# Kernel tuning notes

Hardware: AMD Instinct MI355X
Metric: run time of the kernel (lower is better)

The kernel has to match this reference:

```python
import jax, jax.numpy as jnp
import numpy as np

NEG_SLOPE = 0.1  # negative slope of LeakyReLU in Conv3dReLU/Conv2dReLU


def setup_inputs() -> dict:
    key = jax.random.key(0)
    ks = jax.random.split(key, 16)
    B, C, PREV, N, M1, M2 = 2, 16, 16, 16384, 4096, 4096
    D1, CORR, FILT = 4, 15, 15          # d1 = d+1; (r+1)^d1 - r^d1 with r=1
    CO0, CO1 = 32, 32                    # num_corr_output
    O0, O1 = 64, 64                      # num_output
    CIN = 2 * C + PREV                   # corr_conv input channels

    feat1 = jax.random.normal(ks[0], (B, C, M1), jnp.float32)
    feat2 = jax.random.normal(ks[1], (B, C, M2), jnp.float32)
    prev_corr_feat = jax.random.normal(ks[2], (B, PREV, N), jnp.float32)
    barycentric1 = jax.random.uniform(ks[3], (B, D1, N), jnp.float32)
    # lattice_offset1: batch-offset flattened indices into [0, B*(M1+1)); value -1+1=0 is the pad slot
    local = jax.random.randint(ks[4], (B, D1, N), 0, M1)
    lattice_offset1 = local + (jnp.arange(B, dtype=jnp.int64) * (M1 + 1))[:, None, None]
    pc1_corr_indices = jax.random.randint(ks[5], (B, CORR, M1), -1, M1).astype(jnp.int64)
    pc2_corr_indices = jax.random.randint(ks[6], (B, FILT, CORR, M1), -1, M2).astype(jnp.int64)

    s = 0.05
    cw0 = jax.random.normal(ks[7], (CO0, CIN, CORR), jnp.float32) * s   # Conv3d (1,corr_size,1)
    cb0 = jax.random.normal(ks[8], (CO0,), jnp.float32) * s
    cw1 = jax.random.normal(ks[9], (CO1, CO0), jnp.float32) * s        # Conv3d 1x1x1
    cb1 = jax.random.normal(ks[10], (CO1,), jnp.float32) * s
    bw0 = jax.random.normal(ks[11], (O0, CO1, FILT), jnp.float32) * s  # Conv2d (filter_size,1)
    bb0 = jax.random.normal(ks[12], (O0,), jnp.float32) * s
    bw1 = jax.random.normal(ks[13], (O1, O0), jnp.float32) * s         # Conv2d 1x1 (no relu)
    bb1 = jax.random.normal(ks[14], (O1,), jnp.float32) * s

    return {
        "feat1": feat1, "feat2": feat2, "prev_corr_feat": prev_corr_feat,
        "barycentric1": barycentric1,
        "cw0": cw0, "cb0": cb0, "cw1": cw1, "cb1": cb1,
        "bw0": bw0, "bb0": bb0, "bw1": bw1, "bb1": bb1,
        "lattice_offset1": lattice_offset1,
        "pc1_corr_indices": pc1_corr_indices,
        "pc2_corr_indices": pc2_corr_indices,
        "max_hash_cnt1": M1, "max_hash_cnt2": M2,
    }


def reference(feat1, feat2, prev_corr_feat, barycentric1,
              cw0, cb0, cw1, cb1, bw0, bb0, bw1, bb1,
              lattice_offset1, pc1_corr_indices, pc2_corr_indices,
              max_hash_cnt1, max_hash_cnt2):
    B, C, M1 = feat1.shape
    PREV = prev_corr_feat.shape[1]

    # ---- splat prev_corr_feat onto lattice vertices (scatter-add) ----
    flat_idx = (lattice_offset1 + 1).reshape(-1)                      # (B*d1*N,)
    # (B, PREV, d1, N) -> (B, d1, N, PREV) -> (B*d1*N, PREV)
    vals = (barycentric1[:, None, :, :] * prev_corr_feat[:, :, None, :])
    vals = vals.transpose(0, 2, 3, 1).reshape(-1, PREV)
    prev_splat = jax.ops.segment_sum(vals, flat_idx, num_segments=B * (M1 + 1))
    prev_splat = prev_splat.reshape(B, M1 + 1, PREV).transpose(0, 2, 1)  # (B, PREV, M1+1)

    # use_norm: normalize by splatted barycentric mass
    ones_splat = jax.ops.segment_sum(barycentric1.reshape(-1), flat_idx,
                                     num_segments=B * (M1 + 1)).reshape(B, M1 + 1)
    prev_splat = prev_splat * (1.0 / (ones_splat + 1e-5))[:, None, :]

    # ---- prepend zero pad slot (index 0 catches -1 neighbor indices) ----
    splat1 = jnp.concatenate([prev_splat, jnp.pad(feat1, ((0, 0), (0, 0), (1, 0)))], axis=1)  # (B, PREV+C, M1+1)
    splat2 = jnp.pad(feat2, ((0, 0), (0, 0), (1, 0)))                                          # (B, C, M2+1)

    # ---- irregular gathers ----
    g1 = jax.vmap(lambda s, i: s[:, i])(splat1, pc1_corr_indices + 1)   # (B, PREV+C, corr, M1)
    g2 = jax.vmap(lambda s, i: s[:, i])(splat2, pc2_corr_indices + 1)   # (B, C, filt, corr, M1)
    FILT = g2.shape[2]
    g1b = jnp.broadcast_to(g1[:, :, None], (B, g1.shape[1], FILT, g1.shape[2], M1))
    combined = jnp.concatenate([g1b, g2], axis=1)                       # (B, 2C+PREV, filt, corr, M1)

    # ---- corr_conv: Conv3d(1,corr,1)+LeakyReLU, then 1x1x1+LeakyReLU ----
    x = jnp.einsum('bifkn,oik->bofn', combined, cw0) + cb0[None, :, None, None]
    x = jax.nn.leaky_relu(x, NEG_SLOPE)
    x = jnp.einsum('bcfn,oc->bofn', x, cw1) + cb1[None, :, None, None]
    x = jax.nn.leaky_relu(x, NEG_SLOPE)

    # ---- blur_conv: Conv2d(filt,1)+LeakyReLU, then 1x1 (last_relu=False) ----
    y = jnp.einsum('bcfn,ocf->bon', x, bw0) + bb0[None, :, None]
    y = jax.nn.leaky_relu(y, NEG_SLOPE)
    y = jnp.einsum('bcn,oc->bon', y, bw1) + bb1[None, :, None]
    return y
```

## Files before the change

kernel.cpp:

```cpp
#include <hip/hip_runtime.h>
#include <hip/hip_bf16.h>

namespace {

constexpr int B     = 2;
constexpr int C     = 16;
constexpr int PREVC = 16;
constexpr int NPTS  = 16384;
constexpr int M1    = 4096;
constexpr int D1    = 4;
constexpr int CORR  = 15;
constexpr int FILT  = 15;
constexpr int CIN   = 48;
constexpr int CO0   = 32;
constexpr int O1    = 64;
constexpr int MS    = M1 + 1;
constexpr int NSLOT = B * MS;
constexpr int NPAIR = B * D1 * NPTS;
constexpr int BCAP  = 64;
constexpr int GSTR  = 240;
constexpr float NEG = 0.1f;

constexpr size_t OFF_SP1   = 0;
constexpr size_t SZ_SP1    = (size_t)NSLOT * 32;
constexpr size_t OFF_SP2   = OFF_SP1 + SZ_SP1;
constexpr size_t SZ_SP2    = (size_t)NSLOT * 16;
constexpr size_t OFF_P     = OFF_SP2 + SZ_SP2;
constexpr size_t SZ_PQ     = (size_t)B * CORR * MS * 32 / 2;
constexpr size_t OFF_Q     = OFF_P + SZ_PQ;
constexpr size_t OFF_CWT   = OFF_Q + SZ_PQ;
constexpr size_t SZ_CWT    = (size_t)CORR * CIN * 32;
constexpr size_t OFF_W0R   = OFF_CWT + SZ_CWT;
constexpr size_t SZ_W0R    = 512 * 64;
constexpr size_t OFF_PREVT = OFF_W0R + SZ_W0R;
constexpr size_t SZ_PREVT  = (size_t)B * NPTS * 16;
constexpr size_t OFF_CNT   = OFF_PREVT + SZ_PREVT;
constexpr size_t SZ_CNT    = 8208;
constexpr size_t OFF_REC   = OFF_CNT + SZ_CNT;
constexpr size_t SZ_REC    = (size_t)NSLOT * BCAP;
constexpr size_t OFF_GT    = OFF_REC + SZ_REC;
constexpr size_t SZ_GT     = (size_t)B * M1 * GSTR;

__device__ __forceinline__ float leaky(float v) { return v > 0.f ? v : NEG * v; }
__device__ __forceinline__ float bflo(unsigned u) { return __uint_as_float(u << 16); }
__device__ __forceinline__ float bfhi(unsigned u) { return __uint_as_float(u & 0xffff0000u); }

__global__ __launch_bounds__(256) void k_pre(const int* __restrict__ lo,
                                             const float* __restrict__ prev,
                                             const float* __restrict__ cw0,
                                             const float* __restrict__ bw0,
                                             const int* __restrict__ pc1,
                                             const int* __restrict__ pc2,
                                             int* __restrict__ counts,
                                             int* __restrict__ rec,
                                             float* __restrict__ prevT,
                                             float* __restrict__ cwT,
                                             float* __restrict__ W0r,
                                             unsigned int* __restrict__ gT) {
  int bx = blockIdx.x, tid = threadIdx.x;
  if (bx < 512) {
    int t = bx * 256 + tid;
    int slot = lo[t] + 1;
    int pos = atomicAdd(counts + slot, 1);
    if (pos < BCAP) rec[slot * BCAP + pos] = t;
  } else if (bx < 1024) {
    __shared__ float tile[16][65];
    int bb = bx - 512;
    int b = bb >> 8, n0 = (bb & 255) * 64;
    for (int e = tid; e < 1024; e += 256) {
      int ln = e & 63, r = e >> 6;
      tile[r][ln] = prev[((size_t)b * PREVC + r) * NPTS + n0 + ln];
    }
    __syncthreads();
    for (int e = tid; e < 1024; e += 256) {
      int c = e & 15, nn = e >> 4;
      prevT[((size_t)b * NPTS + n0 + nn) * 16 + c] = tile[c][nn];
    }
  } else if (bx < 1243) {
    int e = (bx - 1024) * 256 + tid;
    if (e < CORR * CIN * 32) {
      int o = e & 31, i = (e >> 5) % CIN, k = e / (CIN * 32);
      cwT[e] = cw0[((size_t)o * CIN + i) * CORR + k];
    }
    int e2 = e - CORR * CIN * 32;
    if (e2 >= 0 && e2 < 512 * 64) {
      int o3 = e2 & 63, cf = e2 >> 6, c = cf >> 4, f = cf & 15;
      W0r[e2] = (f < FILT) ? bw0[((size_t)o3 * CO0 + c) * FILT + f] : 0.f;
    }
  } else {
    __shared__ int tile[16][65];
    int t = bx - 1243;
    int n0 = (t & 63) * 64;
    int rest = t >> 6;
    int b = rest & 1;
    int rt = rest >> 1;
    const int* src; int r0, nr, doff;
    if (rt < 15) { src = pc2 + (size_t)b * FILT * CORR * M1; r0 = rt * 16;
                   nr = min(16, FILT * CORR - r0); doff = 0; }
    else         { src = pc1 + (size_t)b * CORR * M1; r0 = 0; nr = CORR; doff = 225; }
    for (int e = tid; e < nr * 64; e += 256) {
      int ln = e & 63, r = e >> 6;
      tile[r][ln] = src[(size_t)(r0 + r) * M1 + n0 + ln] + 1;
    }
    __syncthreads();
    for (int e = tid; e < 1024; e += 256) {
      int rr = e & 15, nn = e >> 4;
      if (rr < nr)
        gT[((size_t)b * M1 + n0 + nn) * GSTR + doff + r0 + rr] =
            (unsigned int)(tile[rr][nn] * 64);
    }
  }
}

__global__ __launch_bounds__(256) void k_sum(const int* __restrict__ rec,
                                             const int* __restrict__ counts,
                                             const float* __restrict__ bary,
                                             const float* __restrict__ prevT,
                                             const float* __restrict__ feat1,
                                             const float* __restrict__ feat2,
                                             float* __restrict__ splat1,
                                             float* __restrict__ splat2) {
  int tid = threadIdx.x;
  int s = blockIdx.x * 4 + (tid >> 6);
  if (s >= NSLOT) return;
  int lane = tid & 63, c = lane & 15, g = lane >> 4;
  int cnt = min(counts[s], BCAP);
  const int* bucket = rec + (size_t)s * BCAP;
  float acc = 0.f, wsum = 0.f;
  for (int e = g; e < cnt; e += 4) {
    int t = bucket[e];
    float w = bary[t];
    int n = t & (NPTS - 1);
    int b = t >> 16;
    acc += w * prevT[((size_t)b * NPTS + n) * 16 + c];
    wsum += w;
  }
  acc  += __shfl_down(acc, 32);  acc  += __shfl_down(acc, 16);
  wsum += __shfl_down(wsum, 32); wsum += __shfl_down(wsum, 16);
  if (lane < 16) {
    int m = s % MS, b2 = s / MS;
    float scale = 1.f / (wsum + 1e-5f);
    splat1[(size_t)s * 32 + c] = acc * scale;
    float f1 = (m == 0) ? 0.f : feat1[((size_t)b2 * C + c) * M1 + (m - 1)];
    splat1[(size_t)s * 32 + 16 + c] = f1;
    float f2 = (m == 0) ? 0.f : feat2[((size_t)b2 * C + c) * M1 + (m - 1)];
    splat2[(size_t)s * 16 + c] = f2;
  }
}

__global__ __launch_bounds__(256) void k_pq(const float* __restrict__ sp1,
                                            const float* __restrict__ sp2,
                                            const float* __restrict__ cwT,
                                            __hip_bfloat16* __restrict__ Pt,
                                            __hip_bfloat16* __restrict__ Qt) {
  __shared__ float wk[CIN][33];
  int k = blockIdx.y, b = blockIdx.z;
  int tid = threadIdx.x;
  int m = blockIdx.x * 16 + (tid >> 4);
  int o2 = tid & 15;
  for (int e = tid; e < CIN * 32; e += 256)
    wk[e >> 5][e & 31] = cwT[(size_t)k * CIN * 32 + e];
  __syncthreads();
  if (m >= MS) return;
  const float* s1 = sp1 + ((size_t)b * MS + m) * 32;
  const float* s2 = sp2 + ((size_t)b * MS + m) * 16;
  int oa = o2 * 2, ob = oa + 1;
  float q0 = 0, q1 = 0, p0 = 0, p1 = 0;
#pragma unroll
  for (int i4 = 0; i4 < 8; ++i4) {
    float4 s = *(const float4*)(s1 + i4 * 4);
    q0 += s.x * wk[i4*4+0][oa] + s.y * wk[i4*4+1][oa] + s.z * wk[i4*4+2][oa] + s.w * wk[i4*4+3][oa];
    q1 += s.x * wk[i4*4+0][ob] + s.y * wk[i4*4+1][ob] + s.z * wk[i4*4+2][ob] + s.w * wk[i4*4+3][ob];
  }
#pragma unroll
  for (int i4 = 0; i4 < 4; ++i4) {
    float4 s = *(const float4*)(s2 + i4 * 4);
    p0 += s.x * wk[32+i4*4+0][oa] + s.y * wk[32+i4*4+1][oa] + s.z * wk[32+i4*4+2][oa] + s.w * wk[32+i4*4+3][oa];
    p1 += s.x * wk[32+i4*4+0][ob] + s.y * wk[32+i4*4+1][ob] + s.z * wk[32+i4*4+2][ob] + s.w * wk[32+i4*4+3][ob];
  }
  size_t base = ((size_t)(b * CORR + k) * MS + m) * 32;
  __hip_bfloat162 qq, pp;
  qq.x = __float2bfloat16(q0); qq.y = __float2bfloat16(q1);
  pp.x = __float2bfloat16(p0); pp.y = __float2bfloat16(p1);
  *reinterpret_cast<__hip_bfloat162*>(Qt + base + oa) = qq;
  *reinterpret_cast<__hip_bfloat162*>(Pt + base + oa) = pp;
}

__global__ __launch_bounds__(256, 4) void k_gather(const __hip_bfloat16* __restrict__ Pt,
                                                   const __hip_bfloat16* __restrict__ Qt,
                                                   const unsigned int* __restrict__ gT,
                                                   const float* __restrict__ cw1,
                                                   const float* __restrict__ cb0,
                                                   const float* __restrict__ cb1,
                                                   const float* __restrict__ W0r,
                                                   const float* __restrict__ bb0,
                                                   const float* __restrict__ bw1,
                                                   const float* __restrict__ bb1,
                                                   float* __restrict__ out) {
  __shared__ __attribute__((aligned(16))) char smem[19072];
  unsigned int* idxs = (unsigned int*)smem;
  float* parts       = (float*)smem;
  float* p1s         = (float*)(smem + 4096);
  float* xls         = (float*)(smem + 4608);
  float* wch         = (float*)(smem + 4608);
  __hip_bfloat16* hT = (__hip_bfloat16*)(smem + 13824);
  float* y0s         = (float*)(smem + 17984);

  int bid = blockIdx.x;
  int b = (bid >> 2) & 1;
  int r = bid & 3, x = bid >> 3;
  int n0 = (r << 10) | (x << 2);
  int pt0 = (b << 12) | n0;
  int tid = threadIdx.x;

  for (int e = tid; e < 240; e += 256) {
    int pl = e / 60, d = e - pl * 60;
    ((uint4*)(idxs + pl * GSTR))[d] =
        ((const uint4*)(gT + (size_t)(pt0 + pl) * GSTR))[d];
  }
  __syncthreads();

  int pl = tid >> 6, lane = tid & 63;

  {
    int f = lane >> 2, o4 = lane & 3;
    const char* base = (const char*)((f < CORR ? Pt : Qt) + (size_t)b * CORR * MS * 32);
    const unsigned int* ip = idxs + pl * GSTR + (f < CORR ? f * CORR : 225);
    unsigned int lo = (unsigned int)(o4 * 16);
    float a[8] = {};
#pragma unroll
    for (int k = 0; k < CORR; ++k) {
      unsigned int off = ip[k] + (unsigned int)(k * MS * 64) + lo;
      uint4 d = *(const uint4*)(base + off);
      a[0] += bflo(d.x); a[1] += bfhi(d.x);
      a[2] += bflo(d.y); a[3] += bfhi(d.y);
      a[4] += bflo(d.z); a[5] += bfhi(d.z);
      a[6] += bflo(d.w); a[7] += bfhi(d.w);
    }
    if (f == CORR) {
#pragma unroll
      for (int j = 0; j < 8; ++j)
        p1s[pl * 32 + o4 * 8 + j] = a[j] + cb0[o4 * 8 + j];
    }
    __syncthreads();
    if (f < CORR) {
#pragma unroll
      for (int j = 0; j < 8; ++j)
        xls[pl * 576 + f * 36 + o4 * 8 + j] = leaky(a[j] + p1s[pl * 32 + o4 * 8 + j]);
    }
  }
  __syncthreads();

  {
    int o = lane & 31, fh = lane >> 5;
    const float* wrow = cw1 + o * CO0;
    float bias = cb1[o];
    float h[8];
#pragma unroll
    for (int j = 0; j < 8; ++j) {
      float hh = bias;
#pragma unroll
      for (int c4 = 0; c4 < 8; ++c4) {
        float4 xv = *(const float4*)&xls[pl * 576 + (fh * 8 + j) * 36 + c4 * 4];
        float4 w  = *(const float4*)(wrow + c4 * 4);
        hh += w.x * xv.x + w.y * xv.y + w.z * xv.z + w.w * xv.w;
      }
      h[j] = leaky(hh);
    }
    if (fh == 1) h[7] = 0.f;
    union { __hip_bfloat16 hb[8]; uint4 u; } pk;
#pragma unroll
    for (int j = 0; j < 8; ++j) pk.hb[j] = __float2bfloat16(h[j]);
    *(uint4*)(hT + pl * 520 + o * 16 + fh * 8) = pk.u;
  }

  int og = tid & 15, bpl = (tid >> 4) & 3, rep = tid >> 6;
  float acc[4] = {};
  for (int kc = 0; kc < 512; kc += 32) {
    __syncthreads();
    for (int e = tid; e < 512; e += 256) {
      int rr = e >> 4, c4 = e & 15;
      *(float4*)&wch[rr * 68 + c4 * 4] = *(const float4*)(W0r + (size_t)(kc + rr) * 64 + c4 * 4);
    }
    __syncthreads();
#pragma unroll
    for (int i = 0; i < 8; ++i) {
      int kk = rep + i * 4;
      float hv = __bfloat162float(hT[bpl * 520 + kc + kk]);
      float4 w = *(const float4*)&wch[kk * 68 + og * 4];
      acc[0] += w.x * hv; acc[1] += w.y * hv; acc[2] += w.z * hv; acc[3] += w.w * hv;
    }
  }
  __syncthreads();
  *(float4*)&parts[((rep * 4 + bpl) * 16 + og) * 4] = make_float4(acc[0], acc[1], acc[2], acc[3]);
  __syncthreads();

  {
    int ypl = tid & 3, yo3 = tid >> 2;
    int og2 = yo3 >> 2, comp = yo3 & 3;
    float y0 = bb0[yo3];
#pragma unroll
    for (int rp = 0; rp < 4; ++rp)
      y0 += parts[((rp * 4 + ypl) * 16 + og2) * 4 + comp];
    y0s[ypl * 68 + yo3] = leaky(y0);
  }
  __syncthreads();

  {
    int fpl = tid & 3, fo1 = tid >> 2;
    const float* w1row = bw1 + fo1 * 64;
    float y1 = bb1[fo1];
#pragma unroll
    for (int c4 = 0; c4 < 16; ++c4) {
      float4 w = *(const float4*)(w1row + c4 * 4);
      y1 += w.x * y0s[fpl * 68 + c4 * 4 + 0] + w.y * y0s[fpl * 68 + c4 * 4 + 1] +
            w.z * y0s[fpl * 68 + c4 * 4 + 2] + w.w * y0s[fpl * 68 + c4 * 4 + 3];
    }
    out[((size_t)(b * O1 + fo1)) * M1 + n0 + fpl] = y1;
  }
}

}

extern "C" void kernel_launch(void* const* d_in, const int* in_sizes, int n_in,
                              void* d_out, int out_size, void* d_ws, size_t ws_size,
                              hipStream_t stream) {
  const float* feat1 = (const float*)d_in[0];
  const float* feat2 = (const float*)d_in[1];
  const float* prev  = (const float*)d_in[2];
  const float* bary  = (const float*)d_in[3];
  const float* cw0   = (const float*)d_in[4];
  const float* cb0   = (const float*)d_in[5];
  const float* cw1   = (const float*)d_in[6];
  const float* cb1   = (const float*)d_in[7];
  const float* bw0   = (const float*)d_in[8];
  const float* bb0   = (const float*)d_in[9];
  const float* bw1   = (const float*)d_in[10];
  const float* bb1   = (const float*)d_in[11];
  const int* lo  = (const int*)d_in[12];
  const int* pc1 = (const int*)d_in[13];
  const int* pc2 = (const int*)d_in[14];

  float* ws = (float*)d_ws;
  float* splat1 = ws + OFF_SP1;
  float* splat2 = ws + OFF_SP2;
  __hip_bfloat16* Pt = (__hip_bfloat16*)(ws + OFF_P);
  __hip_bfloat16* Qt = (__hip_bfloat16*)(ws + OFF_Q);
  float* cwT   = ws + OFF_CWT;
  float* W0r   = ws + OFF_W0R;
  float* prevT = ws + OFF_PREVT;
  int* counts  = (int*)(ws + OFF_CNT);
  int* rec     = (int*)(ws + OFF_REC);
  unsigned int* gT = (unsigned int*)(ws + OFF_GT);
  float* out   = (float*)d_out;

  hipMemsetAsync(counts, 0, NSLOT * sizeof(int), stream);

  hipLaunchKernelGGL(k_pre, dim3(1243 + 2048), dim3(256), 0, stream,
                     lo, prev, cw0, bw0, pc1, pc2, counts, rec, prevT, cwT, W0r, gT);
  hipLaunchKernelGGL(k_sum, dim3((NSLOT + 3) / 4), dim3(256), 0, stream,
                     rec, counts, bary, prevT, feat1, feat2, splat1, splat2);
  hipLaunchKernelGGL(k_pq, dim3((MS + 15) / 16, CORR, B), dim3(256), 0, stream,
                     splat1, splat2, cwT, Pt, Qt);
  hipLaunchKernelGGL(k_gather, dim3(B * M1 / 4), dim3(256), 0, stream,
                     Pt, Qt, gT, cw1, cb0, cb1, W0r, bb0, bw1, bb1, out);
}
```

Baseline: 112.8 us.

## Shrink gather indices to 16-bit, loop corr in k_pq, read W0r directly

Gather indices are stored as 16-bit values and scaled by 64 in the gather kernel instead of being pre-scaled 32-bit, which halves the index table traffic. k_pq now stages each block's splat rows in shared memory once and loops over all CORR weight slices, rather than launching one block per slice and re-reading the splat rows each time. The blur-conv GEMV in k_gather drops its chunked shared-memory staging of W0r with its barriers and reads weights straight from global memory (cache) with vectorized bf16 unpacking. In exchange, k_pq has fewer, longer blocks and the weight reads in k_gather depend on cache hits.

```diff
diff --git a/kernel.cpp b/kernel.cpp
--- a/kernel.cpp
+++ b/kernel.cpp
@@ -39,7 +39,7 @@
 constexpr size_t OFF_REC   = OFF_CNT + SZ_CNT;
 constexpr size_t SZ_REC    = (size_t)NSLOT * BCAP;
 constexpr size_t OFF_GT    = OFF_REC + SZ_REC;
-constexpr size_t SZ_GT     = (size_t)B * M1 * GSTR;
+constexpr size_t SZ_GT     = (size_t)B * M1 * GSTR / 2;
 
 __device__ __forceinline__ float leaky(float v) { return v > 0.f ? v : NEG * v; }
 __device__ __forceinline__ float bflo(unsigned u) { return __uint_as_float(u << 16); }
@@ -56,7 +56,7 @@
                                              float* __restrict__ prevT,
                                              float* __restrict__ cwT,
                                              float* __restrict__ W0r,
-                                             unsigned int* __restrict__ gT) {
+                                             unsigned short* __restrict__ gT) {
   int bx = blockIdx.x, tid = threadIdx.x;
   if (bx < 512) {
     int t = bx * 256 + tid;
@@ -107,7 +107,7 @@
       int rr = e & 15, nn = e >> 4;
       if (rr < nr)
         gT[((size_t)b * M1 + n0 + nn) * GSTR + doff + r0 + rr] =
-            (unsigned int)(tile[rr][nn] * 64);
+            (unsigned short)tile[rr][nn];
     }
   }
 }
@@ -153,42 +153,54 @@
                                             const float* __restrict__ cwT,
                                             __hip_bfloat16* __restrict__ Pt,
                                             __hip_bfloat16* __restrict__ Qt) {
+  __shared__ float s1s[16][33];
+  __shared__ float s2s[16][17];
   __shared__ float wk[CIN][33];
-  int k = blockIdx.y, b = blockIdx.z;
+  int b = blockIdx.y;
   int tid = threadIdx.x;
-  int m = blockIdx.x * 16 + (tid >> 4);
-  int o2 = tid & 15;
-  for (int e = tid; e < CIN * 32; e += 256)
-    wk[e >> 5][e & 31] = cwT[(size_t)k * CIN * 32 + e];
-  __syncthreads();
-  if (m >= MS) return;
-  const float* s1 = sp1 + ((size_t)b * MS + m) * 32;
-  const float* s2 = sp2 + ((size_t)b * MS + m) * 16;
+  int m0 = blockIdx.x * 16;
+  int mm = tid >> 4, o2 = tid & 15;
+  int m = m0 + mm;
+  for (int e = tid; e < 512; e += 256) {
+    int r = e >> 5, i = e & 31;
+    s1s[r][i] = (m0 + r < MS) ? sp1[((size_t)b * MS + m0 + r) * 32 + i] : 0.f;
+  }
+  {
+    int r = tid >> 4, i = tid & 15;
+    s2s[r][i] = (m0 + r < MS) ? sp2[((size_t)b * MS + m0 + r) * 16 + i] : 0.f;
+  }
+  bool valid = (m < MS);
   int oa = o2 * 2, ob = oa + 1;
-  float q0 = 0, q1 = 0, p0 = 0, p1 = 0;
-#pragma unroll
-  for (int i4 = 0; i4 < 8; ++i4) {
-    float4 s = *(const float4*)(s1 + i4 * 4);
-    q0 += s.x * wk[i4*4+0][oa] + s.y * wk[i4*4+1][oa] + s.z * wk[i4*4+2][oa] + s.w * wk[i4*4+3][oa];
-    q1 += s.x * wk[i4*4+0][ob] + s.y * wk[i4*4+1][ob] + s.z * wk[i4*4+2][ob] + s.w * wk[i4*4+3][ob];
-  }
-#pragma unroll
-  for (int i4 = 0; i4 < 4; ++i4) {
-    float4 s = *(const float4*)(s2 + i4 * 4);
-    p0 += s.x * wk[32+i4*4+0][oa] + s.y * wk[32+i4*4+1][oa] + s.z * wk[32+i4*4+2][oa] + s.w * wk[32+i4*4+3][oa];
-    p1 += s.x * wk[32+i4*4+0][ob] + s.y * wk[32+i4*4+1][ob] + s.z * wk[32+i4*4+2][ob] + s.w * wk[32+i4*4+3][ob];
-  }
-  size_t base = ((size_t)(b * CORR + k) * MS + m) * 32;
-  __hip_bfloat162 qq, pp;
-  qq.x = __float2bfloat16(q0); qq.y = __float2bfloat16(q1);
-  pp.x = __float2bfloat16(p0); pp.y = __float2bfloat16(p1);
-  *reinterpret_cast<__hip_bfloat162*>(Qt + base + oa) = qq;
-  *reinterpret_cast<__hip_bfloat162*>(Pt + base + oa) = pp;
+  for (int k = 0; k < CORR; ++k) {
+    __syncthreads();
+    for (int e = tid; e < CIN * 32; e += 256)
+      wk[e >> 5][e & 31] = cwT[(size_t)k * CIN * 32 + e];
+    __syncthreads();
+    if (valid) {
+      float q0 = 0, q1 = 0, p0 = 0, p1 = 0;
+#pragma unroll
+      for (int i = 0; i < 32; ++i) {
+        float s = s1s[mm][i];
+        q0 += s * wk[i][oa]; q1 += s * wk[i][ob];
+      }
+#pragma unroll
+      for (int i = 0; i < 16; ++i) {
+        float s = s2s[mm][i];
+        p0 += s * wk[32 + i][oa]; p1 += s * wk[32 + i][ob];
+      }
+      size_t base = ((size_t)(b * CORR + k) * MS + m) * 32;
+      __hip_bfloat162 qq, pp;
+      qq.x = __float2bfloat16(q0); qq.y = __float2bfloat16(q1);
+      pp.x = __float2bfloat16(p0); pp.y = __float2bfloat16(p1);
+      *reinterpret_cast<__hip_bfloat162*>(Qt + base + oa) = qq;
+      *reinterpret_cast<__hip_bfloat162*>(Pt + base + oa) = pp;
+    }
+  }
 }
 
 __global__ __launch_bounds__(256, 4) void k_gather(const __hip_bfloat16* __restrict__ Pt,
                                                    const __hip_bfloat16* __restrict__ Qt,
-                                                   const unsigned int* __restrict__ gT,
+                                                   const unsigned short* __restrict__ gT,
                                                    const float* __restrict__ cw1,
                                                    const float* __restrict__ cb0,
                                                    const float* __restrict__ cb1,
@@ -198,11 +210,10 @@
                                                    const float* __restrict__ bb1,
                                                    float* __restrict__ out) {
   __shared__ __attribute__((aligned(16))) char smem[19072];
-  unsigned int* idxs = (unsigned int*)smem;
+  unsigned short* idxs = (unsigned short*)smem;
   float* parts       = (float*)smem;
   float* p1s         = (float*)(smem + 4096);
   float* xls         = (float*)(smem + 4608);
-  float* wch         = (float*)(smem + 4608);
   __hip_bfloat16* hT = (__hip_bfloat16*)(smem + 13824);
   float* y0s         = (float*)(smem + 17984);
 
@@ -213,8 +224,8 @@
   int pt0 = (b << 12) | n0;
   int tid = threadIdx.x;
 
-  for (int e = tid; e < 240; e += 256) {
-    int pl = e / 60, d = e - pl * 60;
+  for (int e = tid; e < 120; e += 256) {
+    int pl = e / 30, d = e - pl * 30;
     ((uint4*)(idxs + pl * GSTR))[d] =
         ((const uint4*)(gT + (size_t)(pt0 + pl) * GSTR))[d];
   }
@@ -225,12 +236,12 @@
   {
     int f = lane >> 2, o4 = lane & 3;
     const char* base = (const char*)((f < CORR ? Pt : Qt) + (size_t)b * CORR * MS * 32);
-    const unsigned int* ip = idxs + pl * GSTR + (f < CORR ? f * CORR : 225);
+    const unsigned short* ip = idxs + pl * GSTR + (f < CORR ? f * CORR : 225);
     unsigned int lo = (unsigned int)(o4 * 16);
     float a[8] = {};
 #pragma unroll
     for (int k = 0; k < CORR; ++k) {
-      unsigned int off = ip[k] + (unsigned int)(k * MS * 64) + lo;
+      unsigned int off = ((unsigned int)ip[k] << 6) + (unsigned int)(k * MS * 64) + lo;
       uint4 d = *(const uint4*)(base + off);
       a[0] += bflo(d.x); a[1] += bfhi(d.x);
       a[2] += bflo(d.y); a[3] += bfhi(d.y);
@@ -273,22 +284,27 @@
     for (int j = 0; j < 8; ++j) pk.hb[j] = __float2bfloat16(h[j]);
     *(uint4*)(hT + pl * 520 + o * 16 + fh * 8) = pk.u;
   }
+  __syncthreads();
 
   int og = tid & 15, bpl = (tid >> 4) & 3, rep = tid >> 6;
   float acc[4] = {};
-  for (int kc = 0; kc < 512; kc += 32) {
-    __syncthreads();
-    for (int e = tid; e < 512; e += 256) {
-      int rr = e >> 4, c4 = e & 15;
-      *(float4*)&wch[rr * 68 + c4 * 4] = *(const float4*)(W0r + (size_t)(kc + rr) * 64 + c4 * 4);
-    }
-    __syncthreads();
-#pragma unroll
-    for (int i = 0; i < 8; ++i) {
-      int kk = rep + i * 4;
-      float hv = __bfloat162float(hT[bpl * 520 + kc + kk]);
-      float4 w = *(const float4*)&wch[kk * 68 + og * 4];
-      acc[0] += w.x * hv; acc[1] += w.y * hv; acc[2] += w.z * hv; acc[3] += w.w * hv;
+  {
+    const __hip_bfloat16* hrow = hT + bpl * 520 + rep * 128;
+    const float* wbase = W0r + (size_t)rep * 128 * 64 + og * 4;
+#pragma unroll 4
+    for (int t8 = 0; t8 < 16; ++t8) {
+      uint4 hp = *(const uint4*)(hrow + t8 * 8);
+      float hv[8];
+      hv[0] = bflo(hp.x); hv[1] = bfhi(hp.x);
+      hv[2] = bflo(hp.y); hv[3] = bfhi(hp.y);
+      hv[4] = bflo(hp.z); hv[5] = bfhi(hp.z);
+      hv[6] = bflo(hp.w); hv[7] = bfhi(hp.w);
+#pragma unroll
+      for (int j = 0; j < 8; ++j) {
+        float4 w = *(const float4*)(wbase + (size_t)(t8 * 8 + j) * 64);
+        acc[0] += w.x * hv[j]; acc[1] += w.y * hv[j];
+        acc[2] += w.z * hv[j]; acc[3] += w.w * hv[j];
+      }
     }
   }
   __syncthreads();
@@ -351,7 +367,7 @@
   float* prevT = ws + OFF_PREVT;
   int* counts  = (int*)(ws + OFF_CNT);
   int* rec     = (int*)(ws + OFF_REC);
-  unsigned int* gT = (unsigned int*)(ws + OFF_GT);
+  unsigned short* gT = (unsigned short*)(ws + OFF_GT);
   float* out   = (float*)d_out;
 
   hipMemsetAsync(counts, 0, NSLOT * sizeof(int), stream);
@@ -360,7 +376,7 @@
                      lo, prev, cw0, bw0, pc1, pc2, counts, rec, prevT, cwT, W0r, gT);
   hipLaunchKernelGGL(k_sum, dim3((NSLOT + 3) / 4), dim3(256), 0, stream,
                      rec, counts, bary, prevT, feat1, feat2, splat1, splat2);
-  hipLaunchKernelGGL(k_pq, dim3((MS + 15) / 16, CORR, B), dim3(256), 0, stream,
+  hipLaunchKernelGGL(k_pq, dim3((MS + 15) / 16, B), dim3(256), 0, stream,
                      splat1, splat2, cwT, Pt, Qt);
   hipLaunchKernelGGL(k_gather, dim3(B * M1 / 4), dim3(256), 0, stream,
                      Pt, Qt, gT, cw1, cb0, cb1, W0r, bb0, bw1, bb1, out);
```

Result: slower. 137.0 us (+21.5%).
